# Kernel optimization log

Hardware: AMD Instinct MI355X
Metric: run time of the kernel (lower is better)

## Reference

```python
import jax, jax.numpy as jnp
import numpy as np

N = 50000   # nodes
E = 800000  # edges
IN_DIM = 512
HID = 256   # total hidden (4 heads x 64)
HEADS = 4
OUT_DIM = 256
NEG_SLOPE = 0.2


def setup_inputs() -> dict:
    key = jax.random.key(0)
    ks = jax.random.split(key, 16)
    s = 0.05
    d = {
        "feats": jax.random.normal(ks[0], (N, IN_DIM), jnp.float32),
        "src": jax.random.randint(ks[1], (E,), 0, N, jnp.int32),
        "dst": jax.random.randint(ks[2], (E,), 0, N, jnp.int32),
        # layer 0: in 512 -> 4 heads x 64
        "W0": jax.random.normal(ks[3], (IN_DIM, HID), jnp.float32) * s,
        "al0": jax.random.normal(ks[4], (HEADS, HID // HEADS), jnp.float32) * s,
        "ar0": jax.random.normal(ks[5], (HEADS, HID // HEADS), jnp.float32) * s,
        "b0": jnp.zeros((HID,), jnp.float32),
        # layer 1: in 256 -> 4 heads x 64
        "W1": jax.random.normal(ks[6], (HID, HID), jnp.float32) * s,
        "al1": jax.random.normal(ks[7], (HEADS, HID // HEADS), jnp.float32) * s,
        "ar1": jax.random.normal(ks[8], (HEADS, HID // HEADS), jnp.float32) * s,
        "b1": jnp.zeros((HID,), jnp.float32),
        # layer 2: in 256 -> 1 head x 256, no activation
        "W2": jax.random.normal(ks[9], (HID, OUT_DIM), jnp.float32) * s,
        "al2": jax.random.normal(ks[10], (1, OUT_DIM), jnp.float32) * s,
        "ar2": jax.random.normal(ks[11], (1, OUT_DIM), jnp.float32) * s,
        "b2": jnp.zeros((OUT_DIM,), jnp.float32),
    }
    return d


def gat_conv(h, src, dst, W, al, ar, b, act):
    """DGL-style GATConv (no dropout, no residual). Returns [N, H, D]."""
    H, D = al.shape
    feat = (h @ W).reshape(-1, H, D)                       # [N,H,D]
    el = jnp.einsum('nhd,hd->nh', feat, al)                # [N,H]
    er = jnp.einsum('nhd,hd->nh', feat, ar)                # [N,H]
    e = jax.nn.leaky_relu(el[src] + er[dst], NEG_SLOPE)    # [E,H]
    # edge softmax over incoming edges per destination node
    m = jax.ops.segment_max(e, dst, num_segments=N)        # [N,H]
    ex = jnp.exp(e - m[dst])                               # [E,H]
    s = jax.ops.segment_sum(ex, dst, num_segments=N)       # [N,H]
    alpha = ex / s[dst]                                    # [E,H]
    msg = jax.ops.segment_sum(alpha[:, :, None] * feat[src], dst, num_segments=N)  # [N,H,D]
    out = msg + b.reshape(1, H, D)
    return act(out) if act is not None else out


def reference(feats, src, dst, W0, al0, ar0, b0, W1, al1, ar1, b1, W2, al2, ar2, b2):
    h = gat_conv(feats, src, dst, W0, al0, ar0, b0, jax.nn.relu)
    h = h.reshape(h.shape[0], -1)                          # flatten heads
    h = gat_conv(h, src, dst, W1, al1, ar1, b1, jax.nn.relu)
    h = h.reshape(h.shape[0], -1)
    h = gat_conv(h, src, dst, W2, al2, ar2, b2, None)
    h = h.mean(axis=1)                                     # last layer: mean over (single) head
    return h
```

## Files before the change

### kernel.cpp

```cpp
#include <hip/hip_runtime.h>
#include <hip/hip_bf16.h>
#include <math.h>


#define HID 256

typedef __attribute__((ext_vector_type(8))) __bf16 bf16x8;
typedef __attribute__((ext_vector_type(4))) __bf16 bf16x4;
typedef __attribute__((ext_vector_type(8))) _Float16 half8;
typedef __attribute__((ext_vector_type(4))) _Float16 half4;
typedef __attribute__((ext_vector_type(4))) float floatx4;

__device__ __forceinline__ void gl_lds16(const void* g, void* l) {
    __builtin_amdgcn_global_load_lds(
        (const __attribute__((address_space(1))) void*)g,
        (__attribute__((address_space(3))) void*)l, 16, 0, 0);
}


__global__ void hist_kernel(const int* __restrict__ dst, int* __restrict__ cnt, int E) {
    int e = blockIdx.x * blockDim.x + threadIdx.x;
    if (e < E) atomicAdd(&cnt[dst[e]], 1);
}

__global__ __launch_bounds__(256) void scan1_kernel(const int* __restrict__ cnt,
                                                    int* __restrict__ bsum, int n) {
    __shared__ int w[4];
    int t = threadIdx.x;
    int i = blockIdx.x * 256 + t;
    int c = (i < n) ? cnt[i] : 0;
    int acc = c;
#pragma unroll
    for (int off = 32; off > 0; off >>= 1) acc += __shfl_xor(acc, off);
    if ((t & 63) == 0) w[t >> 6] = acc;
    __syncthreads();
    if (t == 0) bsum[blockIdx.x] = w[0] + w[1] + w[2] + w[3];
}

__global__ __launch_bounds__(256) void scan2_kernel(const int* __restrict__ bsum,
                                                    int* __restrict__ boff, int nb) {
    __shared__ int buf[256];
    int t = threadIdx.x;
    int v = (t < nb) ? bsum[t] : 0;
    buf[t] = v;
    __syncthreads();
    for (int off = 1; off < 256; off <<= 1) {
        int x = (t >= off) ? buf[t - off] : 0;
        __syncthreads();
        buf[t] += x;
        __syncthreads();
    }
    if (t < nb) boff[t] = buf[t] - v;
}

__global__ __launch_bounds__(256) void scan3_kernel(const int* __restrict__ cnt,
                                                    const int* __restrict__ boff,
                                                    int* __restrict__ rowptr,
                                                    int* __restrict__ cursor, int n) {
    __shared__ int buf[256];
    int t = threadIdx.x;
    int i = blockIdx.x * 256 + t;
    int c = (i < n) ? cnt[i] : 0;
    buf[t] = c;
    __syncthreads();
    for (int off = 1; off < 256; off <<= 1) {
        int x = (t >= off) ? buf[t - off] : 0;
        __syncthreads();
        buf[t] += x;
        __syncthreads();
    }
    int start = boff[blockIdx.x] + buf[t] - c;
    if (i < n) {
        rowptr[i] = start;
        cursor[i] = start;
        if (i == n - 1) rowptr[n] = start + c;
    }
}

__global__ void fill_kernel(const int* __restrict__ src, const int* __restrict__ dst,
                            int* __restrict__ cursor, int* __restrict__ adj, int E) {
    int e = blockIdx.x * blockDim.x + threadIdx.x;
    if (e < E) {
        int d = dst[e];
        int pos = atomicAdd(&cursor[d], 1);
        adj[pos] = src[e];
    }
}


__global__ __launch_bounds__(256) void split_kernel(const float* __restrict__ x,
                                                    __bf16* __restrict__ hi,
                                                    __bf16* __restrict__ lo, int n4) {
    int i = blockIdx.x * blockDim.x + threadIdx.x;
    if (i < n4) {
        float4 v = ((const float4*)x)[i];
        float vv[4] = {v.x, v.y, v.z, v.w};
        bf16x4 h, l;
#pragma unroll
        for (int c = 0; c < 4; c++) {
            __bf16 hh = (__bf16)vv[c];
            h[c] = hh;
            l[c] = (__bf16)(vv[c] - (float)hh);
        }
        ((bf16x4*)hi)[i] = h;
        ((bf16x4*)lo)[i] = l;
    }
}

__global__ __launch_bounds__(256) void splitT_kernel(const float* __restrict__ B,
                                                     __bf16* __restrict__ ht,
                                                     __bf16* __restrict__ lt,
                                                     int K, int Nn) {
    int i = blockIdx.x * blockDim.x + threadIdx.x;
    if (i < K * Nn) {
        int k = i / Nn, n = i - k * Nn;
        float v = B[i];
        __bf16 h = (__bf16)v;
        __bf16 l = (__bf16)(v - (float)h);
        ht[(size_t)n * K + k] = h;
        lt[(size_t)n * K + k] = l;
    }
}


__global__ __launch_bounds__(256, 2) void gemm_mfma_kernel(
    const __bf16* __restrict__ Ah, const __bf16* __restrict__ Al,
    const __bf16* __restrict__ Bht, const __bf16* __restrict__ Blt,
    _Float16* __restrict__ C, int M, int K) {
    __shared__ __bf16 sAh[128 * 32];
    __shared__ __bf16 sAl[128 * 32];
    __shared__ __bf16 sBh[128 * 32];
    __shared__ __bf16 sBl[128 * 32];

    int t = threadIdx.x;
    int wave = t >> 6, lane = t & 63;
    int wr = wave >> 1, wc = wave & 1;
    int quad = lane >> 4, m16 = lane & 15;

    int rowA0 = blockIdx.y * 128;
    int rowB0 = blockIdx.x * 128;

    int sr = t >> 2;
    int ke = (t & 3) * 8;
    int ldso = t * 8;

    size_t ar0 = (size_t)min(rowA0 + sr, M - 1) * K;
    size_t ar1 = (size_t)min(rowA0 + sr + 64, M - 1) * K;
    size_t br0 = (size_t)(rowB0 + sr) * K;
    size_t br1 = (size_t)(rowB0 + sr + 64) * K;

    floatx4 acc[4][4];
    floatx4 z = {0.f, 0.f, 0.f, 0.f};
#pragma unroll
    for (int i = 0; i < 4; i++)
#pragma unroll
        for (int j = 0; j < 4; j++) acc[i][j] = z;

    int nk = K >> 5;
    for (int kt = 0; kt < nk; kt++) {
        int k0 = (kt << 5) + ke;
        gl_lds16(Ah + ar0 + k0, &sAh[ldso]);
        gl_lds16(Ah + ar1 + k0, &sAh[2048 + ldso]);
        gl_lds16(Al + ar0 + k0, &sAl[ldso]);
        gl_lds16(Al + ar1 + k0, &sAl[2048 + ldso]);
        gl_lds16(Bht + br0 + k0, &sBh[ldso]);
        gl_lds16(Bht + br1 + k0, &sBh[2048 + ldso]);
        gl_lds16(Blt + br0 + k0, &sBl[ldso]);
        gl_lds16(Blt + br1 + k0, &sBl[2048 + ldso]);
        __syncthreads();

        bf16x8 fah[4], fal[4], fbh[4], fbl[4];
#pragma unroll
        for (int i = 0; i < 4; i++) {
            int off = (wr * 64 + i * 16 + m16) * 32 + quad * 8;
            fah[i] = *(const bf16x8*)&sAh[off];
            fal[i] = *(const bf16x8*)&sAl[off];
        }
#pragma unroll
        for (int j = 0; j < 4; j++) {
            int off = (wc * 64 + j * 16 + m16) * 32 + quad * 8;
            fbh[j] = *(const bf16x8*)&sBh[off];
            fbl[j] = *(const bf16x8*)&sBl[off];
        }
#pragma unroll
        for (int i = 0; i < 4; i++)
#pragma unroll
            for (int j = 0; j < 4; j++) {
                acc[i][j] = __builtin_amdgcn_mfma_f32_16x16x32_bf16(fah[i], fbh[j], acc[i][j], 0, 0, 0);
                acc[i][j] = __builtin_amdgcn_mfma_f32_16x16x32_bf16(fah[i], fbl[j], acc[i][j], 0, 0, 0);
                acc[i][j] = __builtin_amdgcn_mfma_f32_16x16x32_bf16(fal[i], fbh[j], acc[i][j], 0, 0, 0);
            }
        __syncthreads();
    }

#pragma unroll
    for (int i = 0; i < 4; i++) {
        int rowb = rowA0 + wr * 64 + i * 16 + quad * 4;
#pragma unroll
        for (int j = 0; j < 4; j++) {
            int col = rowB0 + wc * 64 + j * 16 + m16;
#pragma unroll
            for (int r = 0; r < 4; r++) {
                int row = rowb + r;
                if (row < M) C[(size_t)row * HID + col] = (_Float16)acc[i][j][r];
            }
        }
    }
}


__global__ __launch_bounds__(256) void gemm_kernel(const float* __restrict__ A,
                                                   const float* __restrict__ B,
                                                   _Float16* __restrict__ C,
                                                   int M, int K, int Nn) {
    __shared__ float As[16][128];
    __shared__ float Bs[16][128];

    int t = threadIdx.x;
    int tx = t & 15, ty = t >> 4;
    int arow = t >> 1;
    int acol = (t & 1) * 8;
    int brow = t >> 4;
    int bcol = (t & 15) * 8;

    int gArow = blockIdx.y * 128 + arow;
    const float* aPtr = A + (size_t)gArow * K + acol;
    const float* bPtr = B + (size_t)brow * Nn + blockIdx.x * 128 + bcol;

    float acc[8][8];
#pragma unroll
    for (int i = 0; i < 8; i++)
#pragma unroll
        for (int j = 0; j < 8; j++) acc[i][j] = 0.f;

    bool aok = (gArow < M);
    int nk = K >> 4;
    for (int kt = 0; kt < nk; kt++) {
        int k0 = kt << 4;
        float4 av0 = make_float4(0.f, 0.f, 0.f, 0.f), av1 = av0;
        if (aok) {
            av0 = *(const float4*)(aPtr + k0);
            av1 = *(const float4*)(aPtr + k0 + 4);
        }
        float4 bv0 = *(const float4*)(bPtr + (size_t)k0 * Nn);
        float4 bv1 = *(const float4*)(bPtr + (size_t)k0 * Nn + 4);

        As[acol + 0][arow] = av0.x;
        As[acol + 1][arow] = av0.y;
        As[acol + 2][arow] = av0.z;
        As[acol + 3][arow] = av0.w;
        As[acol + 4][arow] = av1.x;
        As[acol + 5][arow] = av1.y;
        As[acol + 6][arow] = av1.z;
        As[acol + 7][arow] = av1.w;
        *(float4*)&Bs[brow][bcol] = bv0;
        *(float4*)&Bs[brow][bcol + 4] = bv1;
        __syncthreads();

#pragma unroll
        for (int kk = 0; kk < 16; kk++) {
            float4 a0 = *(const float4*)&As[kk][ty * 4];
            float4 a1 = *(const float4*)&As[kk][64 + ty * 4];
            float4 b0 = *(const float4*)&Bs[kk][tx * 4];
            float4 b1 = *(const float4*)&Bs[kk][64 + tx * 4];
            float a[8] = {a0.x, a0.y, a0.z, a0.w, a1.x, a1.y, a1.z, a1.w};
            float b[8] = {b0.x, b0.y, b0.z, b0.w, b1.x, b1.y, b1.z, b1.w};
#pragma unroll
            for (int i = 0; i < 8; i++)
#pragma unroll
                for (int j = 0; j < 8; j++) acc[i][j] = fmaf(a[i], b[j], acc[i][j]);
        }
        __syncthreads();
    }

    int c0 = blockIdx.x * 128 + tx * 4;
#pragma unroll
    for (int half = 0; half < 2; half++) {
#pragma unroll
        for (int i = 0; i < 4; i++) {
            int r = blockIdx.y * 128 + half * 64 + ty * 4 + i;
            if (r < M) {
                _Float16* cp = C + (size_t)r * Nn + c0;
                int ai = half * 4 + i;
#pragma unroll
                for (int j = 0; j < 4; j++) {
                    cp[j] = (_Float16)acc[ai][j];
                    cp[64 + j] = (_Float16)acc[ai][4 + j];
                }
            }
        }
    }
}


__global__ __launch_bounds__(256) void elr_kernel(const _Float16* __restrict__ feat,
                                                  const float* __restrict__ al,
                                                  const float* __restrict__ ar,
                                                  float* __restrict__ el,
                                                  float* __restrict__ er, int H) {
    int n = blockIdx.x, t = threadIdx.x;
    float f = (float)feat[(size_t)n * HID + t];
    float a = f * al[t];
    float b = f * ar[t];
#pragma unroll
    for (int off = 32; off > 0; off >>= 1) {
        a += __shfl_xor(a, off);
        b += __shfl_xor(b, off);
    }
    __shared__ float pa[4], pb[4];
    int wave = t >> 6, lane = t & 63;
    if (lane == 0) { pa[wave] = a; pb[wave] = b; }
    __syncthreads();
    if (H == 4) {
        if (t < 4) {
            el[n * 4 + t] = pa[t];
            er[n * 4 + t] = pb[t];
        }
    } else {
        if (t == 0) {
            el[n] = pa[0] + pa[1] + pa[2] + pa[3];
            er[n] = pb[0] + pb[1] + pb[2] + pb[3];
        }
    }
}


template <int H, bool RELU, bool WF32, bool WSPLIT>
__global__ __launch_bounds__(256) void agg_tpl(
    const _Float16* __restrict__ feat, const float* __restrict__ el,
    const float* __restrict__ er, const int* __restrict__ rowptr,
    const int* __restrict__ adj, const float* __restrict__ bias,
    _Float16* __restrict__ exbuf,
    float* __restrict__ outf, __bf16* __restrict__ oh, __bf16* __restrict__ ol,
    int N) {
    int wave = threadIdx.x >> 6, lane = threadIdx.x & 63;
    int v = blockIdx.x * 4 + wave;
    if (v >= N) return;
    int row0 = rowptr[v];
    int deg = rowptr[v + 1] - row0;

    int l32 = lane & 31;
    int half = lane >> 5;
    int hd = (H == 4) ? (l32 >> 3) : 0;
    int d0 = l32 * 8;

    float o[8];
    if (deg > 0) {
        float s[H], er_v[H];
#pragma unroll
        for (int h = 0; h < H; h++) {
            er_v[h] = er[v * H + h];
            s[h] = 0.f;
        }

        for (int e = lane; e < deg; e += 64) {
            int u = adj[row0 + e];
            if (H == 4) {
                float4 elu = *(const float4*)&el[u * 4];
                float ev[4] = {elu.x, elu.y, elu.z, elu.w};
                half4 exq;
#pragma unroll
                for (int h = 0; h < 4; h++) {
                    float sc = ev[h] + er_v[h];
                    sc = (sc > 0.f) ? sc : 0.2f * sc;
                    float ex = __expf(sc);
                    s[h] += ex;
                    exq[h] = (_Float16)ex;
                }
                *(half4*)&exbuf[(size_t)(row0 + e) * 4] = exq;
            } else {
                float sc = el[u] + er_v[0];
                sc = (sc > 0.f) ? sc : 0.2f * sc;
                float ex = __expf(sc);
                s[0] += ex;
                exbuf[row0 + e] = (_Float16)ex;
            }
        }
#pragma unroll
        for (int h = 0; h < H; h++)
#pragma unroll
            for (int off = 32; off > 0; off >>= 1) s[h] += __shfl_xor(s[h], off);

        __threadfence_block();

        float s_l = (H == 4) ? ((l32 & 16) ? ((l32 & 8) ? s[3] : s[2])
                                           : ((l32 & 8) ? s[1] : s[0]))
                             : s[0];
        float inv_l = 1.f / s_l;

        const _Float16* exb = exbuf + (size_t)row0 * H;
        const int* adjr = adj + row0;

        float a[8];
#pragma unroll
        for (int j = 0; j < 8; j++) a[j] = 0.f;

        int e = 0;
        for (; e + 8 <= deg; e += 8) {
            int u[4];
            float alp[4];
            half8 f[4];
#pragma unroll
            for (int q = 0; q < 4; q++) {
                int ee = e + q * 2 + half;
                u[q] = adjr[ee];
                alp[q] = (float)exb[ee * H + hd];
            }
#pragma unroll
            for (int q = 0; q < 4; q++)
                f[q] = *(const half8*)&feat[(size_t)u[q] * HID + d0];
#pragma unroll
            for (int q = 0; q < 4; q++) {
                float al_ = alp[q] * inv_l;
#pragma unroll
                for (int j = 0; j < 8; j++) a[j] = fmaf(al_, (float)f[q][j], a[j]);
            }
        }
        for (; e < deg; e += 2) {
            int ee = e + half;
            bool act = ee < deg;
            int es = act ? ee : (deg - 1);
            int u = adjr[es];
            float al_ = act ? ((float)exb[es * H + hd] * inv_l) : 0.f;
            half8 f = *(const half8*)&feat[(size_t)u * HID + d0];
#pragma unroll
            for (int j = 0; j < 8; j++) a[j] = fmaf(al_, (float)f[j], a[j]);
        }
#pragma unroll
        for (int j = 0; j < 8; j++) a[j] += __shfl_xor(a[j], 32);

#pragma unroll
        for (int j = 0; j < 8; j++) {
            o[j] = a[j] + bias[d0 + j];
            if (RELU) o[j] = fmaxf(o[j], 0.f);
        }
    } else {
#pragma unroll
        for (int j = 0; j < 8; j++) {
            o[j] = bias[d0 + j];
            if (RELU) o[j] = fmaxf(o[j], 0.f);
        }
    }

    if (half == 0) {
        size_t base = (size_t)v * HID + d0;
        if (WF32) {
            *(float4*)&outf[base] = make_float4(o[0], o[1], o[2], o[3]);
            *(float4*)&outf[base + 4] = make_float4(o[4], o[5], o[6], o[7]);
        }
        if (WSPLIT) {
            bf16x8 hh, ll;
#pragma unroll
            for (int j = 0; j < 8; j++) {
                __bf16 hv = (__bf16)o[j];
                hh[j] = hv;
                ll[j] = (__bf16)(o[j] - (float)hv);
            }
            *(bf16x8*)&oh[base] = hh;
            *(bf16x8*)&ol[base] = ll;
        }
    }
}


extern "C" void kernel_launch(void* const* d_in, const int* in_sizes, int n_in,
                              void* d_out, int out_size, void* d_ws, size_t ws_size,
                              hipStream_t stream) {
    const float* feats = (const float*)d_in[0];
    const int* src = (const int*)d_in[1];
    const int* dst = (const int*)d_in[2];
    const float* W0 = (const float*)d_in[3];
    const float* al0 = (const float*)d_in[4];
    const float* ar0 = (const float*)d_in[5];
    const float* b0 = (const float*)d_in[6];
    const float* W1 = (const float*)d_in[7];
    const float* al1 = (const float*)d_in[8];
    const float* ar1 = (const float*)d_in[9];
    const float* b1 = (const float*)d_in[10];
    const float* W2 = (const float*)d_in[11];
    const float* al2 = (const float*)d_in[12];
    const float* ar2 = (const float*)d_in[13];
    const float* b2 = (const float*)d_in[14];
    float* out = (float*)d_out;

    const int IN_DIM = 512;
    const int N = in_sizes[0] / IN_DIM;
    const int E = in_sizes[1];

    char* ws = (char*)d_ws;
    size_t off = 0;
    auto alloc = [&](size_t bytes) -> void* {
        void* p = ws + off;
        off = (off + bytes + 255) & ~(size_t)255;
        return p;
    };
    _Float16* featbuf = (_Float16*)alloc((size_t)N * HID * sizeof(_Float16));
    float* el = (float*)alloc((size_t)N * 4 * sizeof(float));
    float* er = (float*)alloc((size_t)N * 4 * sizeof(float));
    int* cnt = (int*)alloc((size_t)N * sizeof(int));
    int* rowptr = (int*)alloc((size_t)(N + 1) * sizeof(int));
    int* cursor = (int*)alloc((size_t)N * sizeof(int));
    int* adj = (int*)alloc((size_t)E * sizeof(int));
    _Float16* exbuf = (_Float16*)alloc((size_t)E * 4 * sizeof(_Float16));
    int nscanb = (N + 255) / 256;
    int* bsum = (int*)alloc((size_t)nscanb * sizeof(int));
    int* boff = (int*)alloc((size_t)nscanb * sizeof(int));
    __bf16* Ah = (__bf16*)alloc((size_t)N * 512 * sizeof(__bf16));
    __bf16* Al = (__bf16*)alloc((size_t)N * 512 * sizeof(__bf16));
    __bf16* Bht = (__bf16*)alloc((size_t)512 * HID * sizeof(__bf16));
    __bf16* Blt = (__bf16*)alloc((size_t)512 * HID * sizeof(__bf16));
    bool use_mfma = (off <= ws_size);

    hipMemsetAsync(cnt, 0, (size_t)N * sizeof(int), stream);
    hist_kernel<<<(E + 255) / 256, 256, 0, stream>>>(dst, cnt, E);
    scan1_kernel<<<nscanb, 256, 0, stream>>>(cnt, bsum, N);
    scan2_kernel<<<1, 256, 0, stream>>>(bsum, boff, nscanb);
    scan3_kernel<<<nscanb, 256, 0, stream>>>(cnt, boff, rowptr, cursor, N);
    fill_kernel<<<(E + 255) / 256, 256, 0, stream>>>(src, dst, cursor, adj, E);

    dim3 ggrid(HID / 128, (N + 127) / 128);
    int aggb = (N + 3) / 4;

    if (use_mfma) {
        split_kernel<<<(N * 512 / 4 + 255) / 256, 256, 0, stream>>>(feats, Ah, Al, N * 512 / 4);
        splitT_kernel<<<(512 * HID + 255) / 256, 256, 0, stream>>>(W0, Bht, Blt, 512, HID);
        gemm_mfma_kernel<<<ggrid, 256, 0, stream>>>(Ah, Al, Bht, Blt, featbuf, N, 512);
        elr_kernel<<<N, 256, 0, stream>>>(featbuf, al0, ar0, el, er, 4);
        agg_tpl<4, true, false, true><<<aggb, 256, 0, stream>>>(
            featbuf, el, er, rowptr, adj, b0, exbuf, nullptr, Ah, Al, N);

        splitT_kernel<<<(256 * HID + 255) / 256, 256, 0, stream>>>(W1, Bht, Blt, 256, HID);
        gemm_mfma_kernel<<<ggrid, 256, 0, stream>>>(Ah, Al, Bht, Blt, featbuf, N, 256);
        elr_kernel<<<N, 256, 0, stream>>>(featbuf, al1, ar1, el, er, 4);
        agg_tpl<4, true, false, true><<<aggb, 256, 0, stream>>>(
            featbuf, el, er, rowptr, adj, b1, exbuf, nullptr, Ah, Al, N);

        splitT_kernel<<<(256 * HID + 255) / 256, 256, 0, stream>>>(W2, Bht, Blt, 256, HID);
        gemm_mfma_kernel<<<ggrid, 256, 0, stream>>>(Ah, Al, Bht, Blt, featbuf, N, 256);
        elr_kernel<<<N, 256, 0, stream>>>(featbuf, al2, ar2, el, er, 1);
        agg_tpl<1, false, true, false><<<aggb, 256, 0, stream>>>(
            featbuf, el, er, rowptr, adj, b2, exbuf, out, nullptr, nullptr, N);
    } else {
        gemm_kernel<<<ggrid, 256, 0, stream>>>(feats, W0, featbuf, N, 512, HID);
        elr_kernel<<<N, 256, 0, stream>>>(featbuf, al0, ar0, el, er, 4);
        agg_tpl<4, true, true, false><<<aggb, 256, 0, stream>>>(
            featbuf, el, er, rowptr, adj, b0, exbuf, out, nullptr, nullptr, N);

        gemm_kernel<<<ggrid, 256, 0, stream>>>(out, W1, featbuf, N, 256, HID);
        elr_kernel<<<N, 256, 0, stream>>>(featbuf, al1, ar1, el, er, 4);
        agg_tpl<4, true, true, false><<<aggb, 256, 0, stream>>>(
            featbuf, el, er, rowptr, adj, b1, exbuf, out, nullptr, nullptr, N);

        gemm_kernel<<<ggrid, 256, 0, stream>>>(out, W2, featbuf, N, 256, HID);
        elr_kernel<<<N, 256, 0, stream>>>(featbuf, al2, ar2, el, er, 1);
        agg_tpl<1, false, true, false><<<aggb, 256, 0, stream>>>(
            featbuf, el, er, rowptr, adj, b2, exbuf, out, nullptr, nullptr, N);
    }
}
```

Measured before the change: 709.9 us.

## Fuse input bf16 split and attention-logit computation into MFMA GEMM

The layer-0 GEMM now loads fp32 features directly and splits them into hi/lo bf16 in registers before writing to LDS. This removes the standalone split kernel and the large Ah/Al round trip through global memory. The el/er attention logits are computed in the GEMM epilogue with cross-lane shuffles, which removes the three elr kernels; the single-head layer accumulates them with atomics after a memset. The three weight splits are merged into one launch, and the aggregation loop gains a 16-edge unrolled stage for more memory-level parallelism. The trade-off is that layer-0 A loads become synchronous register loads instead of direct-to-LDS loads, and the GEMM epilogue carries extra work and register pressure.

```diff
diff --git a/kernel.cpp b/kernel.cpp
--- a/kernel.cpp
+++ b/kernel.cpp
@@ -88,45 +88,34 @@
 }
 
 
-__global__ __launch_bounds__(256) void split_kernel(const float* __restrict__ x,
-                                                    __bf16* __restrict__ hi,
-                                                    __bf16* __restrict__ lo, int n4) {
-    int i = blockIdx.x * blockDim.x + threadIdx.x;
-    if (i < n4) {
-        float4 v = ((const float4*)x)[i];
-        float vv[4] = {v.x, v.y, v.z, v.w};
-        bf16x4 h, l;
-#pragma unroll
-        for (int c = 0; c < 4; c++) {
-            __bf16 hh = (__bf16)vv[c];
-            h[c] = hh;
-            l[c] = (__bf16)(vv[c] - (float)hh);
-        }
-        ((bf16x4*)hi)[i] = h;
-        ((bf16x4*)lo)[i] = l;
-    }
-}
-
-__global__ __launch_bounds__(256) void splitT_kernel(const float* __restrict__ B,
-                                                     __bf16* __restrict__ ht,
-                                                     __bf16* __restrict__ lt,
-                                                     int K, int Nn) {
-    int i = blockIdx.x * blockDim.x + threadIdx.x;
-    if (i < K * Nn) {
-        int k = i / Nn, n = i - k * Nn;
-        float v = B[i];
-        __bf16 h = (__bf16)v;
-        __bf16 l = (__bf16)(v - (float)h);
-        ht[(size_t)n * K + k] = h;
-        lt[(size_t)n * K + k] = l;
-    }
-}
-
-
+__device__ __forceinline__ void splitT_one(const float* W, __bf16* ht, __bf16* lt,
+                                           int idx, int K) {
+    int k = idx >> 8, n = idx & 255;
+    float v = W[idx];
+    __bf16 h = (__bf16)v;
+    ht[(size_t)n * K + k] = h;
+    lt[(size_t)n * K + k] = (__bf16)(v - (float)h);
+}
+
+__global__ __launch_bounds__(256) void splitT_all_kernel(
+    const float* __restrict__ W0, const float* __restrict__ W1,
+    const float* __restrict__ W2, __bf16* h0, __bf16* l0, __bf16* h1,
+    __bf16* l1, __bf16* h2, __bf16* l2) {
+    int i = blockIdx.x * 256 + threadIdx.x;
+    const int n0 = 512 * 256, n1 = 256 * 256;
+    if (i < n0) splitT_one(W0, h0, l0, i, 512);
+    else if (i < n0 + n1) splitT_one(W1, h1, l1, i - n0, 256);
+    else if (i < n0 + 2 * n1) splitT_one(W2, h2, l2, i - n0 - n1, 256);
+}
+
+
+template <bool SPLITA>
 __global__ __launch_bounds__(256, 2) void gemm_mfma_kernel(
-    const __bf16* __restrict__ Ah, const __bf16* __restrict__ Al,
-    const __bf16* __restrict__ Bht, const __bf16* __restrict__ Blt,
-    _Float16* __restrict__ C, int M, int K) {
+    const float* __restrict__ Af, const __bf16* __restrict__ Ah,
+    const __bf16* __restrict__ Al, const __bf16* __restrict__ Bht,
+    const __bf16* __restrict__ Blt, _Float16* __restrict__ C,
+    const float* __restrict__ al, const float* __restrict__ ar,
+    float* __restrict__ el, float* __restrict__ er, int M, int K, int H) {
     __shared__ __bf16 sAh[128 * 32];
     __shared__ __bf16 sAl[128 * 32];
     __shared__ __bf16 sBh[128 * 32];
@@ -143,9 +132,16 @@
     int sr = t >> 2;
     int ke = (t & 3) * 8;
     int ldso = t * 8;
-
-    size_t ar0 = (size_t)min(rowA0 + sr, M - 1) * K;
-    size_t ar1 = (size_t)min(rowA0 + sr + 64, M - 1) * K;
+    int srow = t >> 1;
+    int kb = (t & 1) * 16;
+
+    size_t ar0 = 0, ar1 = 0, af0 = 0;
+    if (SPLITA) {
+        af0 = (size_t)min(rowA0 + srow, M - 1) * K + kb;
+    } else {
+        ar0 = (size_t)min(rowA0 + sr, M - 1) * K;
+        ar1 = (size_t)min(rowA0 + sr + 64, M - 1) * K;
+    }
     size_t br0 = (size_t)(rowB0 + sr) * K;
     size_t br1 = (size_t)(rowB0 + sr + 64) * K;
 
@@ -158,15 +154,40 @@
 
     int nk = K >> 5;
     for (int kt = 0; kt < nk; kt++) {
-        int k0 = (kt << 5) + ke;
-        gl_lds16(Ah + ar0 + k0, &sAh[ldso]);
-        gl_lds16(Ah + ar1 + k0, &sAh[2048 + ldso]);
-        gl_lds16(Al + ar0 + k0, &sAl[ldso]);
-        gl_lds16(Al + ar1 + k0, &sAl[2048 + ldso]);
-        gl_lds16(Bht + br0 + k0, &sBh[ldso]);
-        gl_lds16(Bht + br1 + k0, &sBh[2048 + ldso]);
-        gl_lds16(Blt + br0 + k0, &sBl[ldso]);
-        gl_lds16(Blt + br1 + k0, &sBl[2048 + ldso]);
+        int k0s = (kt << 5) + ke;
+        gl_lds16(Bht + br0 + k0s, &sBh[ldso]);
+        gl_lds16(Bht + br1 + k0s, &sBh[2048 + ldso]);
+        gl_lds16(Blt + br0 + k0s, &sBl[ldso]);
+        gl_lds16(Blt + br1 + k0s, &sBl[2048 + ldso]);
+        if (SPLITA) {
+            const float* ap = Af + af0 + (kt << 5);
+            float4 v0 = ((const float4*)ap)[0];
+            float4 v1 = ((const float4*)ap)[1];
+            float4 v2 = ((const float4*)ap)[2];
+            float4 v3 = ((const float4*)ap)[3];
+            float vv[16] = {v0.x, v0.y, v0.z, v0.w, v1.x, v1.y, v1.z, v1.w,
+                            v2.x, v2.y, v2.z, v2.w, v3.x, v3.y, v3.z, v3.w};
+            bf16x8 h0, h1, l0, l1;
+#pragma unroll
+            for (int c = 0; c < 8; c++) {
+                __bf16 hv = (__bf16)vv[c];
+                h0[c] = hv;
+                l0[c] = (__bf16)(vv[c] - (float)hv);
+                __bf16 hv2 = (__bf16)vv[8 + c];
+                h1[c] = hv2;
+                l1[c] = (__bf16)(vv[8 + c] - (float)hv2);
+            }
+            int so = srow * 32 + kb;
+            *(bf16x8*)&sAh[so] = h0;
+            *(bf16x8*)&sAh[so + 8] = h1;
+            *(bf16x8*)&sAl[so] = l0;
+            *(bf16x8*)&sAl[so + 8] = l1;
+        } else {
+            gl_lds16(Ah + ar0 + k0s, &sAh[ldso]);
+            gl_lds16(Ah + ar1 + k0s, &sAh[2048 + ldso]);
+            gl_lds16(Al + ar0 + k0s, &sAl[ldso]);
+            gl_lds16(Al + ar1 + k0s, &sAl[2048 + ldso]);
+        }
         __syncthreads();
 
         bf16x8 fah[4], fal[4], fbh[4], fbl[4];
@@ -203,6 +224,41 @@
             for (int r = 0; r < 4; r++) {
                 int row = rowb + r;
                 if (row < M) C[(size_t)row * HID + col] = (_Float16)acc[i][j][r];
+            }
+        }
+    }
+
+    float alv[4], arv[4];
+#pragma unroll
+    for (int j = 0; j < 4; j++) {
+        int col = rowB0 + wc * 64 + j * 16 + m16;
+        alv[j] = al[col];
+        arv[j] = ar[col];
+    }
+    int h = ((rowB0 + wc * 64) >> 6) & (H - 1);
+#pragma unroll
+    for (int i = 0; i < 4; i++) {
+        int rowb = rowA0 + wr * 64 + i * 16 + quad * 4;
+#pragma unroll
+        for (int r = 0; r < 4; r++) {
+            float pe = acc[i][0][r] * alv[0] + acc[i][1][r] * alv[1] +
+                       acc[i][2][r] * alv[2] + acc[i][3][r] * alv[3];
+            float pr = acc[i][0][r] * arv[0] + acc[i][1][r] * arv[1] +
+                       acc[i][2][r] * arv[2] + acc[i][3][r] * arv[3];
+#pragma unroll
+            for (int off = 1; off < 16; off <<= 1) {
+                pe += __shfl_xor(pe, off);
+                pr += __shfl_xor(pr, off);
+            }
+            int row = rowb + r;
+            if (m16 == 0 && row < M) {
+                if (H == 4) {
+                    el[row * 4 + h] = pe;
+                    er[row * 4 + h] = pr;
+                } else {
+                    atomicAdd(&el[row], pe);
+                    atomicAdd(&er[row], pr);
+                }
             }
         }
     }
@@ -396,6 +452,26 @@
         for (int j = 0; j < 8; j++) a[j] = 0.f;
 
         int e = 0;
+        for (; e + 16 <= deg; e += 16) {
+            int u[8];
+            float alp[8];
+            half8 f[8];
+#pragma unroll
+            for (int q = 0; q < 8; q++) {
+                int ee = e + q * 2 + half;
+                u[q] = adjr[ee];
+                alp[q] = (float)exb[ee * H + hd];
+            }
+#pragma unroll
+            for (int q = 0; q < 8; q++)
+                f[q] = *(const half8*)&feat[(size_t)u[q] * HID + d0];
+#pragma unroll
+            for (int q = 0; q < 8; q++) {
+                float al_ = alp[q] * inv_l;
+#pragma unroll
+                for (int j = 0; j < 8; j++) a[j] = fmaf(al_, (float)f[q][j], a[j]);
+            }
+        }
         for (; e + 8 <= deg; e += 8) {
             int u[4];
             float alp[4];
@@ -505,10 +581,14 @@
     int nscanb = (N + 255) / 256;
     int* bsum = (int*)alloc((size_t)nscanb * sizeof(int));
     int* boff = (int*)alloc((size_t)nscanb * sizeof(int));
-    __bf16* Ah = (__bf16*)alloc((size_t)N * 512 * sizeof(__bf16));
-    __bf16* Al = (__bf16*)alloc((size_t)N * 512 * sizeof(__bf16));
-    __bf16* Bht = (__bf16*)alloc((size_t)512 * HID * sizeof(__bf16));
-    __bf16* Blt = (__bf16*)alloc((size_t)512 * HID * sizeof(__bf16));
+    __bf16* Ah = (__bf16*)alloc((size_t)N * HID * sizeof(__bf16));
+    __bf16* Al = (__bf16*)alloc((size_t)N * HID * sizeof(__bf16));
+    __bf16* Bht0 = (__bf16*)alloc((size_t)512 * HID * sizeof(__bf16));
+    __bf16* Blt0 = (__bf16*)alloc((size_t)512 * HID * sizeof(__bf16));
+    __bf16* Bht1 = (__bf16*)alloc((size_t)256 * HID * sizeof(__bf16));
+    __bf16* Blt1 = (__bf16*)alloc((size_t)256 * HID * sizeof(__bf16));
+    __bf16* Bht2 = (__bf16*)alloc((size_t)256 * HID * sizeof(__bf16));
+    __bf16* Blt2 = (__bf16*)alloc((size_t)256 * HID * sizeof(__bf16));
     bool use_mfma = (off <= ws_size);
 
     hipMemsetAsync(cnt, 0, (size_t)N * sizeof(int), stream);
@@ -522,22 +602,22 @@
     int aggb = (N + 3) / 4;
 
     if (use_mfma) {
-        split_kernel<<<(N * 512 / 4 + 255) / 256, 256, 0, stream>>>(feats, Ah, Al, N * 512 / 4);
-        splitT_kernel<<<(512 * HID + 255) / 256, 256, 0, stream>>>(W0, Bht, Blt, 512, HID);
-        gemm_mfma_kernel<<<ggrid, 256, 0, stream>>>(Ah, Al, Bht, Blt, featbuf, N, 512);
-        elr_kernel<<<N, 256, 0, stream>>>(featbuf, al0, ar0, el, er, 4);
+        splitT_all_kernel<<<(512 * 256 + 2 * 256 * 256) / 256, 256, 0, stream>>>(
+            W0, W1, W2, Bht0, Blt0, Bht1, Blt1, Bht2, Blt2);
+
+        gemm_mfma_kernel<true><<<ggrid, 256, 0, stream>>>(
+            feats, nullptr, nullptr, Bht0, Blt0, featbuf, al0, ar0, el, er, N, 512, 4);
         agg_tpl<4, true, false, true><<<aggb, 256, 0, stream>>>(
             featbuf, el, er, rowptr, adj, b0, exbuf, nullptr, Ah, Al, N);
 
-        splitT_kernel<<<(256 * HID + 255) / 256, 256, 0, stream>>>(W1, Bht, Blt, 256, HID);
-        gemm_mfma_kernel<<<ggrid, 256, 0, stream>>>(Ah, Al, Bht, Blt, featbuf, N, 256);
-        elr_kernel<<<N, 256, 0, stream>>>(featbuf, al1, ar1, el, er, 4);
+        gemm_mfma_kernel<false><<<ggrid, 256, 0, stream>>>(
+            nullptr, Ah, Al, Bht1, Blt1, featbuf, al1, ar1, el, er, N, 256, 4);
         agg_tpl<4, true, false, true><<<aggb, 256, 0, stream>>>(
             featbuf, el, er, rowptr, adj, b1, exbuf, nullptr, Ah, Al, N);
 
-        splitT_kernel<<<(256 * HID + 255) / 256, 256, 0, stream>>>(W2, Bht, Blt, 256, HID);
-        gemm_mfma_kernel<<<ggrid, 256, 0, stream>>>(Ah, Al, Bht, Blt, featbuf, N, 256);
-        elr_kernel<<<N, 256, 0, stream>>>(featbuf, al2, ar2, el, er, 1);
+        hipMemsetAsync(el, 0, (size_t)N * 8 * sizeof(float), stream);
+        gemm_mfma_kernel<false><<<ggrid, 256, 0, stream>>>(
+            nullptr, Ah, Al, Bht2, Blt2, featbuf, al2, ar2, el, er, N, 256, 1);
         agg_tpl<1, false, true, false><<<aggb, 256, 0, stream>>>(
             featbuf, el, er, rowptr, adj, b2, exbuf, out, nullptr, nullptr, N);
     } else {
```

Measured after the change: 640.1 us. 9.8% less time.
